# Performance work log

Hardware: AMD Instinct MI355X
Metric: run time of the kernel (lower is better)

Reference implementation:

```python
import jax, jax.numpy as jnp
import numpy as np

N = 8192        # num nodes == input_dim (attn is [N,N], indexed by edge endpoints)
E = 262144      # num edges (nnz of sparse G), avg degree 32
OD = 64         # output_dim


def setup_inputs() -> dict:
    key = jax.random.key(0)
    k_x, k_r, k_c, k_v, k_a, k_w = jax.random.split(key, 6)
    x = jax.random.normal(k_x, (N, N), dtype=jnp.float32)
    row = jax.random.randint(k_r, (E,), 0, N)
    col = jax.random.randint(k_c, (E,), 0, N)
    values = jax.random.uniform(k_v, (E,), dtype=jnp.float32)
    attn = jax.random.uniform(k_a, (N, N), dtype=jnp.float32)  # init uniform(0,1) per reset_parameters
    stdv = 1.0 / np.sqrt(OD)
    weight = jax.random.uniform(k_w, (N, OD), dtype=jnp.float32, minval=-stdv, maxval=stdv)
    return {"x": x, "attn": attn, "weight": weight, "values": values, "row": row, "col": col}


def reference(x, attn, weight, values, row, col):
    # x = x @ W : [N, OD]
    y = x @ weight
    # sparse_dense_mul: scale each edge's value by attn[row, col] (irregular gather)
    ev = values * attn[row, col]                      # [E]
    # torch.sparse.mm(G, y): out[i] = sum_{e: row[e]==i} ev[e] * y[col[e]]
    out = jax.ops.segment_sum(ev[:, None] * y[col], row, num_segments=x.shape[0])
    return (out, jnp.linalg.norm(attn))
```

## Files before the change

### kernel.cpp

```cpp
#include <hip/hip_runtime.h>
#include <hip/hip_bf16.h>

#define N 8192
#define OD 64
#define E_EDGES 262144

#define BM 64
#define KSPLIT 32
#define KSLICE (N / KSPLIT)
#define SCAT_BLOCKS 8192
#define EDGE_ITERS (E_EDGES / (SCAT_BLOCKS * 4))

typedef __attribute__((ext_vector_type(8))) short bf16x8;
typedef __attribute__((ext_vector_type(4))) float f32x4;

__device__ __forceinline__ unsigned short f2bf(float f) {
    union { float f; unsigned u; } v; v.f = f;
    unsigned r = (v.u + 0x7fffu + ((v.u >> 16) & 1u)) >> 16;
    return (unsigned short)r;
}

__device__ __forceinline__ unsigned pack_trunc(unsigned lo, unsigned hi) {
#if defined(__has_builtin) && __has_builtin(__builtin_amdgcn_perm)
    return __builtin_amdgcn_perm(hi, lo, 0x07060302u);
#else
    return (lo >> 16) | (hi & 0xFFFF0000u);
#endif
}

__device__ __forceinline__ void gload16(const void* g, void* l) {
    __builtin_amdgcn_global_load_lds(
        (const __attribute__((address_space(1))) unsigned int*)g,
        (__attribute__((address_space(3))) unsigned int*)l, 16, 0, 0);
}

__global__ __launch_bounds__(256) void prep_kernel(const float* __restrict__ w,
                                                   unsigned short* __restrict__ wt,
                                                   float4* __restrict__ y4,
                                                   float4* __restrict__ out4) {
    const int bid = blockIdx.x, t = threadIdx.x;
    const int base = bid * 256 + t;
    float4 z{0.f, 0.f, 0.f, 0.f};
    #pragma unroll
    for (int u = 0; u < 4; ++u) y4[base + u * 32768] = z;
    #pragma unroll
    for (int u = 0; u < 4; ++u) out4[base + u * 32768] = z;

    __shared__ unsigned short lds[64][80];
    const int kb = bid * 64;
    #pragma unroll
    for (int p = 0; p < 4; ++p) {
        int idx = p * 1024 + t * 4;
        int r = idx >> 6, c = idx & 63;
        float4 v = *(const float4*)(&w[(size_t)(kb + r) * OD + c]);
        lds[c + 0][r] = f2bf(v.x);
        lds[c + 1][r] = f2bf(v.y);
        lds[c + 2][r] = f2bf(v.z);
        lds[c + 3][r] = f2bf(v.w);
    }
    __syncthreads();
    const int colx = t >> 2, j0 = (t & 3) * 16;
    #pragma unroll
    for (int u = 0; u < 2; ++u) {
        *(bf16x8*)(wt + (size_t)colx * N + kb + j0 + u * 8) =
            *(const bf16x8*)(&lds[colx][j0 + u * 8]);
    }
}

__global__ __launch_bounds__(256) void gemm_kernel(const float* __restrict__ x,
                                                   const unsigned short* __restrict__ wt,
                                                   float* __restrict__ y) {
    __shared__ unsigned short blds[64 * KSLICE];

    const int t = threadIdx.x;
    const int wv = t >> 6, lane = t & 63;
    const int lrow = lane & 15, g = lane >> 4;
    const int row = blockIdx.x * BM + wv * 16 + lrow;
    const int k0 = blockIdx.y * KSLICE;
    const int key = (lrow & 7) << 3;

    #pragma unroll
    for (int j = 0; j < 8; ++j) {
        const int idx = j * 256 + t;
        const int br = idx >> 5;
        const int ch = idx & 31;
        gload16(wt + (size_t)br * N + k0 + ((ch ^ (br & 7)) << 3),
                &blds[idx * 8]);
    }
    asm volatile("s_waitcnt vmcnt(0)" ::: "memory");
    __builtin_amdgcn_sched_barrier(0);
    __builtin_amdgcn_s_barrier();

    f32x4 acc[4] = {f32x4{0,0,0,0}, f32x4{0,0,0,0}, f32x4{0,0,0,0}, f32x4{0,0,0,0}};
    const float* xp = x + (size_t)row * N + k0 + g * 8;
    uint4 xb[8];
    bf16x8 A[4];

    #define LOADQ(q)                                                  \
        _Pragma("unroll")                                             \
        for (int i = 0; i < 4; ++i) {                                 \
            xb[2*i]   = *(const uint4*)(xp + (q) * 128 + i * 32);     \
            xb[2*i+1] = *(const uint4*)(xp + (q) * 128 + i * 32 + 4); \
        }

    #define PACKQ()                                                   \
        _Pragma("unroll")                                             \
        for (int i = 0; i < 4; ++i) {                                 \
            union { bf16x8 v; unsigned u[4]; } Au;                    \
            Au.u[0] = pack_trunc(xb[2*i].x,   xb[2*i].y);             \
            Au.u[1] = pack_trunc(xb[2*i].z,   xb[2*i].w);             \
            Au.u[2] = pack_trunc(xb[2*i+1].x, xb[2*i+1].y);           \
            Au.u[3] = pack_trunc(xb[2*i+1].z, xb[2*i+1].w);           \
            A[i] = Au.v;                                              \
        }

    #define MFMAQ(q)                                                               \
        _Pragma("unroll")                                                          \
        for (int ks = 0; ks < 4; ++ks) {                                           \
            _Pragma("unroll")                                                      \
            for (int cf = 0; cf < 4; ++cf) {                                       \
                const int ko = (q) * 128 + ks * 32 + g * 8;                        \
                bf16x8 b = *(const bf16x8*)&blds[(cf * 16 + lrow) * KSLICE +       \
                                                 (ko ^ key)];                      \
                acc[cf] = __builtin_amdgcn_mfma_f32_16x16x32_bf16(A[ks], b,        \
                                                                  acc[cf], 0,0,0); \
            }                                                                      \
        }

    LOADQ(0);
    PACKQ(); LOADQ(1); MFMAQ(0);
    PACKQ();           MFMAQ(1);

    float* yp = y + ((size_t)blockIdx.x * BM + wv * 16 + g * 4) * OD;
    #pragma unroll
    for (int cf = 0; cf < 4; ++cf) {
        #pragma unroll
        for (int i = 0; i < 4; ++i)
            atomicAdd(&yp[i * OD + cf * 16 + lrow], acc[cf][i]);
    }
    #undef LOADQ
    #undef PACKQ
    #undef MFMAQ
}

__device__ __forceinline__ void do_scatter(const float* __restrict__ values,
                                           const float* __restrict__ attn,
                                           const int* __restrict__ row,
                                           const int* __restrict__ col,
                                           const float* __restrict__ y,
                                           float* __restrict__ out,
                                           int bid, int t) {
    const int lane = t & 63;
    const int w = t >> 6;
    int r8[EDGE_ITERS], c8[EDGE_ITERS];
    float v8[EDGE_ITERS], a8[EDGE_ITERS];
    #pragma unroll
    for (int i = 0; i < EDGE_ITERS; ++i) {
        int e = bid * 4 + w + i * (SCAT_BLOCKS * 4);
        r8[i] = row[e]; c8[i] = col[e]; v8[i] = values[e];
    }
    #pragma unroll
    for (int i = 0; i < EDGE_ITERS; ++i)
        a8[i] = attn[(size_t)r8[i] * N + c8[i]];
    #pragma unroll
    for (int i = 0; i < EDGE_ITERS; ++i) {
        float yv = y[c8[i] * OD + lane];
        atomicAdd(&out[r8[i] * OD + lane], v8[i] * a8[i] * yv);
    }
}

__device__ __forceinline__ float do_norm_part(const float* __restrict__ attn, int bid, int t) {
    const float4* a4 = (const float4*)attn;
    float s = 0.f;
    int i = bid * 256 + t;
    #pragma unroll
    for (int u = 0; u < 8; ++u) {
        float4 v = a4[i + u * (SCAT_BLOCKS * 256)];
        s += v.x * v.x + v.y * v.y + v.z * v.z + v.w * v.w;
    }
    return s;
}

__global__ __launch_bounds__(256) void scatter_norm_kernel(
        const float* __restrict__ values, const float* __restrict__ attn,
        const int* __restrict__ row, const int* __restrict__ col,
        const float* __restrict__ y, float* __restrict__ out,
        float* __restrict__ part) {
    const int bid = blockIdx.x, t = threadIdx.x;
    float s;
    if (bid & 1) {
        s = do_norm_part(attn, bid, t);
        do_scatter(values, attn, row, col, y, out, bid, t);
    } else {
        do_scatter(values, attn, row, col, y, out, bid, t);
        s = do_norm_part(attn, bid, t);
    }
    for (int off = 32; off > 0; off >>= 1) s += __shfl_down(s, off, 64);
    __shared__ float wpart[4];
    int wid = t >> 6;
    if ((t & 63) == 0) wpart[wid] = s;
    __syncthreads();
    if (t == 0) part[bid] = wpart[0] + wpart[1] + wpart[2] + wpart[3];
}

__global__ __launch_bounds__(256) void finalize_kernel(const float* __restrict__ part,
                                                       float* __restrict__ out_norm) {
    float s = 0.f;
    #pragma unroll
    for (int k = 0; k < SCAT_BLOCKS / 256; ++k) s += part[k * 256 + threadIdx.x];
    for (int off = 32; off > 0; off >>= 1) s += __shfl_down(s, off, 64);
    __shared__ float wp[4];
    int wid = threadIdx.x >> 6;
    if ((threadIdx.x & 63) == 0) wp[wid] = s;
    __syncthreads();
    if (threadIdx.x == 0) *out_norm = sqrtf(wp[0] + wp[1] + wp[2] + wp[3]);
}

extern "C" void kernel_launch(void* const* d_in, const int* in_sizes, int n_in,
                              void* d_out, int out_size, void* d_ws, size_t ws_size,
                              hipStream_t stream) {
    const float* x      = (const float*)d_in[0];
    const float* attn   = (const float*)d_in[1];
    const float* weight = (const float*)d_in[2];
    const float* values = (const float*)d_in[3];
    const int*   row    = (const int*)d_in[4];
    const int*   col    = (const int*)d_in[5];
    float* out = (float*)d_out;

    char* wsb = (char*)d_ws;
    float*          part = (float*)wsb;
    unsigned short* wt   = (unsigned short*)(wsb + (1u << 20));
    float*          y    = (float*)(wsb + (2u << 20));

    prep_kernel<<<128, 256, 0, stream>>>(weight, wt, (float4*)y, (float4*)out);
    gemm_kernel<<<dim3(N / BM, KSPLIT), 256, 0, stream>>>(x, wt, y);
    scatter_norm_kernel<<<SCAT_BLOCKS, 256, 0, stream>>>(values, attn, row, col, y, out, part);
    finalize_kernel<<<1, 256, 0, stream>>>(part, out + (size_t)N * OD);
}
```

Baseline: 158.0 us.

## Move attn norm into prep kernel and fold finalize into scatter launch

The Frobenius-norm reduction over attn moves out of the scatter kernel and into an enlarged prep kernel with 2048 blocks. That kernel also zeroes y and out and transposes the weight to bf16. The final norm reduction now runs as an extra block of the scatter launch, which drops the separate finalize kernel. The aim is to take the 256MB streaming read off the latency-bound scatter kernel and remove one launch. The cost is that prep is no longer tiny and now sits serially before the GEMM instead of overlapping with scatter.

```diff
diff --git a/kernel.cpp b/kernel.cpp
--- a/kernel.cpp
+++ b/kernel.cpp
@@ -8,6 +8,7 @@
 #define BM 64
 #define KSPLIT 32
 #define KSLICE (N / KSPLIT)
+#define NORM_BLOCKS 2048
 #define SCAT_BLOCKS 8192
 #define EDGE_ITERS (E_EDGES / (SCAT_BLOCKS * 4))
 
@@ -34,37 +35,56 @@
         (__attribute__((address_space(3))) unsigned int*)l, 16, 0, 0);
 }
 
-__global__ __launch_bounds__(256) void prep_kernel(const float* __restrict__ w,
-                                                   unsigned short* __restrict__ wt,
-                                                   float4* __restrict__ y4,
-                                                   float4* __restrict__ out4) {
+__global__ __launch_bounds__(256) void prep_norm_kernel(const float* __restrict__ attn,
+                                                        const float* __restrict__ w,
+                                                        unsigned short* __restrict__ wt,
+                                                        float4* __restrict__ y4,
+                                                        float4* __restrict__ out4,
+                                                        float* __restrict__ part) {
     const int bid = blockIdx.x, t = threadIdx.x;
-    const int base = bid * 256 + t;
-    float4 z{0.f, 0.f, 0.f, 0.f};
-    #pragma unroll
-    for (int u = 0; u < 4; ++u) y4[base + u * 32768] = z;
-    #pragma unroll
-    for (int u = 0; u < 4; ++u) out4[base + u * 32768] = z;
-
-    __shared__ unsigned short lds[64][80];
-    const int kb = bid * 64;
-    #pragma unroll
-    for (int p = 0; p < 4; ++p) {
-        int idx = p * 1024 + t * 4;
-        int r = idx >> 6, c = idx & 63;
-        float4 v = *(const float4*)(&w[(size_t)(kb + r) * OD + c]);
-        lds[c + 0][r] = f2bf(v.x);
-        lds[c + 1][r] = f2bf(v.y);
-        lds[c + 2][r] = f2bf(v.z);
-        lds[c + 3][r] = f2bf(v.w);
-    }
+
+    if (t < 128) {
+        int zi = bid * 128 + t;
+        float4 z{0.f, 0.f, 0.f, 0.f};
+        if (zi < 131072) y4[zi] = z;
+        else out4[zi - 131072] = z;
+    }
+
+    if (bid < 128) {
+        __shared__ unsigned short lds[64][80];
+        const int kb = bid * 64;
+        #pragma unroll
+        for (int p = 0; p < 4; ++p) {
+            int idx = p * 1024 + t * 4;
+            int r = idx >> 6, c = idx & 63;
+            float4 v = *(const float4*)(&w[(size_t)(kb + r) * OD + c]);
+            lds[c + 0][r] = f2bf(v.x);
+            lds[c + 1][r] = f2bf(v.y);
+            lds[c + 2][r] = f2bf(v.z);
+            lds[c + 3][r] = f2bf(v.w);
+        }
+        __syncthreads();
+        const int colx = t >> 2, j0 = (t & 3) * 16;
+        #pragma unroll
+        for (int u = 0; u < 2; ++u) {
+            *(bf16x8*)(wt + (size_t)colx * N + kb + j0 + u * 8) =
+                *(const bf16x8*)(&lds[colx][j0 + u * 8]);
+        }
+    }
+
+    const float4* a4 = (const float4*)attn;
+    const int total = (N * (long)N) / 4;
+    float s = 0.f;
+    for (long i = (long)bid * 256 + t; i < total; i += (long)NORM_BLOCKS * 256) {
+        float4 v = a4[i];
+        s += v.x * v.x + v.y * v.y + v.z * v.z + v.w * v.w;
+    }
+    for (int off = 32; off > 0; off >>= 1) s += __shfl_down(s, off, 64);
+    __shared__ float wpart[4];
+    int wid = t >> 6;
+    if ((t & 63) == 0) wpart[wid] = s;
     __syncthreads();
-    const int colx = t >> 2, j0 = (t & 3) * 16;
-    #pragma unroll
-    for (int u = 0; u < 2; ++u) {
-        *(bf16x8*)(wt + (size_t)colx * N + kb + j0 + u * 8) =
-            *(const bf16x8*)(&lds[colx][j0 + u * 8]);
-    }
+    if (t == 0) part[bid] = wpart[0] + wpart[1] + wpart[2] + wpart[3];
 }
 
 __global__ __launch_bounds__(256) void gemm_kernel(const float* __restrict__ x,
@@ -143,13 +163,28 @@
     #undef MFMAQ
 }
 
-__device__ __forceinline__ void do_scatter(const float* __restrict__ values,
-                                           const float* __restrict__ attn,
-                                           const int* __restrict__ row,
-                                           const int* __restrict__ col,
-                                           const float* __restrict__ y,
-                                           float* __restrict__ out,
-                                           int bid, int t) {
+__global__ __launch_bounds__(256) void scatter_kernel(const float* __restrict__ values,
+                                                      const float* __restrict__ attn,
+                                                      const int* __restrict__ row,
+                                                      const int* __restrict__ col,
+                                                      const float* __restrict__ y,
+                                                      float* __restrict__ out,
+                                                      const float* __restrict__ part,
+                                                      float* __restrict__ out_norm) {
+    const int t = threadIdx.x;
+    if (blockIdx.x == SCAT_BLOCKS) {
+        float s = 0.f;
+        #pragma unroll
+        for (int k = 0; k < NORM_BLOCKS / 256; ++k) s += part[k * 256 + t];
+        for (int off = 32; off > 0; off >>= 1) s += __shfl_down(s, off, 64);
+        __shared__ float wp[4];
+        int wid = t >> 6;
+        if ((t & 63) == 0) wp[wid] = s;
+        __syncthreads();
+        if (t == 0) *out_norm = sqrtf(wp[0] + wp[1] + wp[2] + wp[3]);
+        return;
+    }
+    const int bid = blockIdx.x;
     const int lane = t & 63;
     const int w = t >> 6;
     int r8[EDGE_ITERS], c8[EDGE_ITERS];
@@ -167,53 +202,6 @@
         float yv = y[c8[i] * OD + lane];
         atomicAdd(&out[r8[i] * OD + lane], v8[i] * a8[i] * yv);
     }
-}
-
-__device__ __forceinline__ float do_norm_part(const float* __restrict__ attn, int bid, int t) {
-    const float4* a4 = (const float4*)attn;
-    float s = 0.f;
-    int i = bid * 256 + t;
-    #pragma unroll
-    for (int u = 0; u < 8; ++u) {
-        float4 v = a4[i + u * (SCAT_BLOCKS * 256)];
-        s += v.x * v.x + v.y * v.y + v.z * v.z + v.w * v.w;
-    }
-    return s;
-}
-
-__global__ __launch_bounds__(256) void scatter_norm_kernel(
-        const float* __restrict__ values, const float* __restrict__ attn,
-        const int* __restrict__ row, const int* __restrict__ col,
-        const float* __restrict__ y, float* __restrict__ out,
-        float* __restrict__ part) {
-    const int bid = blockIdx.x, t = threadIdx.x;
-    float s;
-    if (bid & 1) {
-        s = do_norm_part(attn, bid, t);
-        do_scatter(values, attn, row, col, y, out, bid, t);
-    } else {
-        do_scatter(values, attn, row, col, y, out, bid, t);
-        s = do_norm_part(attn, bid, t);
-    }
-    for (int off = 32; off > 0; off >>= 1) s += __shfl_down(s, off, 64);
-    __shared__ float wpart[4];
-    int wid = t >> 6;
-    if ((t & 63) == 0) wpart[wid] = s;
-    __syncthreads();
-    if (t == 0) part[bid] = wpart[0] + wpart[1] + wpart[2] + wpart[3];
-}
-
-__global__ __launch_bounds__(256) void finalize_kernel(const float* __restrict__ part,
-                                                       float* __restrict__ out_norm) {
-    float s = 0.f;
-    #pragma unroll
-    for (int k = 0; k < SCAT_BLOCKS / 256; ++k) s += part[k * 256 + threadIdx.x];
-    for (int off = 32; off > 0; off >>= 1) s += __shfl_down(s, off, 64);
-    __shared__ float wp[4];
-    int wid = threadIdx.x >> 6;
-    if ((threadIdx.x & 63) == 0) wp[wid] = s;
-    __syncthreads();
-    if (threadIdx.x == 0) *out_norm = sqrtf(wp[0] + wp[1] + wp[2] + wp[3]);
 }
 
 extern "C" void kernel_launch(void* const* d_in, const int* in_sizes, int n_in,
@@ -232,8 +220,9 @@
     unsigned short* wt   = (unsigned short*)(wsb + (1u << 20));
     float*          y    = (float*)(wsb + (2u << 20));
 
-    prep_kernel<<<128, 256, 0, stream>>>(weight, wt, (float4*)y, (float4*)out);
+    prep_norm_kernel<<<NORM_BLOCKS, 256, 0, stream>>>(attn, weight, wt, (float4*)y,
+                                                      (float4*)out, part);
     gemm_kernel<<<dim3(N / BM, KSPLIT), 256, 0, stream>>>(x, wt, y);
-    scatter_norm_kernel<<<SCAT_BLOCKS, 256, 0, stream>>>(values, attn, row, col, y, out, part);
-    finalize_kernel<<<1, 256, 0, stream>>>(part, out + (size_t)N * OD);
-}
+    scatter_kernel<<<SCAT_BLOCKS + 1, 256, 0, stream>>>(values, attn, row, col, y, out,
+                                                        part, out + (size_t)N * OD);
+}
```

Result: slower. 174.0 us (+10.1%).
